# Kernel optimization log

Hardware: AMD Instinct MI355X
Metric: run time of the kernel (lower is better)

## Reference

```python
import jax, jax.numpy as jnp
import numpy as np

GENES = 20000   # input gene nodes (depth 0)
LEVEL = 10000   # nodes per subsequent depth level
STEPS = 7       # depth propagation steps
DEG = 16        # in-degree per dst node
N = GENES + STEPS * LEVEL          # 90000 total nodes
EPS = LEVEL * DEG                  # 160000 edges per step
E = STEPS * EPS                    # 1120000 total edges
B = 256
C = 2


def setup_inputs() -> dict:
    key = jax.random.key(0)
    k0, k1, k2 = jax.random.split(key, 3)
    X = jax.random.normal(k0, (B, GENES), jnp.float32)
    gene_map = jnp.arange(GENES, dtype=jnp.int32)

    rng = np.random.default_rng(0)
    src_list, dstu_list = [], []
    for k in range(STEPS):
        lo = 0 if k == 0 else GENES + (k - 1) * LEVEL
        hi = GENES if k == 0 else lo + LEVEL
        src_list.append(rng.integers(lo, hi, size=EPS))
        dstu_list.append(np.arange(GENES + k * LEVEL, GENES + (k + 1) * LEVEL))
    src = jnp.asarray(np.stack(src_list), dtype=jnp.int32)          # [STEPS, EPS]
    dst_unique = jnp.asarray(np.stack(dstu_list), dtype=jnp.int32)  # [STEPS, LEVEL]
    dst_pos = jnp.tile(jnp.repeat(jnp.arange(LEVEL, dtype=jnp.int32), DEG)[None, :], (STEPS, 1))
    eid = jnp.arange(E, dtype=jnp.int32).reshape(STEPS, EPS)
    root_ids = dst_unique[-1]

    edge_weight = jax.random.normal(k1, (E,), jnp.float32) * 0.01
    node_bias = jnp.zeros((N,), jnp.float32)
    head_W = jax.random.normal(k2, (LEVEL, C), jnp.float32) * (1.0 / np.sqrt(LEVEL))
    head_b = jnp.zeros((C,), jnp.float32)

    return dict(X=X, edge_weight=edge_weight, node_bias=node_bias,
                head_W=head_W, head_b=head_b, gene_map=gene_map,
                src=src, dst_pos=dst_pos, dst_unique=dst_unique,
                eid=eid, root_ids=root_ids)


def reference(X, edge_weight, node_bias, head_W, head_b,
              gene_map, src, dst_pos, dst_unique, eid, root_ids):
    # dropout is identity (eval mode / p=0)
    b = X.shape[0]
    h = jnp.zeros((b, N), X.dtype).at[:, gene_map].set(X)
    for k in range(src.shape[0]):  # fixed small number of depth steps
        w = edge_weight[eid[k]]                                   # [EPS]
        msg = h[:, src[k]] * w[None, :]                           # gather + scale [B, EPS]
        agg = jnp.zeros((b, dst_unique.shape[1]), h.dtype).at[:, dst_pos[k]].add(msg)
        h_dst = jnp.tanh(agg + node_bias[dst_unique[k]][None, :])  # [B, LEVEL]
        h = h.at[:, dst_unique[k]].set(h_dst)
    roots = h[:, root_ids]                                        # [B, LEVEL]
    return roots @ head_W + head_b
```

## Files before the change

kernel.cpp:

```cpp
#include <hip/hip_runtime.h>
#include <math.h>

#define GENES 20000
#define LEVEL 10000
#define STEPS 7
#define DEG   16
#define EPSZ  (LEVEL * DEG)
#define CCOLS 32
#define NCHUNK 8
#define SBLK  157
#define NGT   625
#define MSTRIDE 18

typedef unsigned short bf8 __attribute__((ext_vector_type(8)));

__device__ inline float bf2f(unsigned short u) {
    union { unsigned u; float f; } c; c.u = ((unsigned)u) << 16; return c.f;
}
__device__ inline unsigned short f2bf(float x) {
    union { float f; unsigned u; } c; c.f = x;
    return (unsigned short)((c.u + 0x7fffu + ((c.u >> 16) & 1u)) >> 16);
}

__global__ __launch_bounds__(256) void transpose_k(const float* __restrict__ X,
                                                   const int*   __restrict__ gene_map,
                                                   unsigned short* __restrict__ XT) {
    __shared__ float tile[32][33];
    const int chunk = blockIdx.x;
    const int lo = threadIdx.x & 31, r = threadIdx.x >> 5;
    unsigned short* XTp = XT + (size_t)chunk * GENES * CCOLS;
    for (int i = 0; i < 4; ++i) {
        const int gt = blockIdx.y * 4 + i;
        if (gt >= NGT) break;
        const int g0 = gt * 32;
        if (i) __syncthreads();
#pragma unroll
        for (int j = 0; j < 4; ++j) {
            const int b = r + j * 8;
            tile[b][lo] = X[(size_t)(chunk * CCOLS + b) * GENES + g0 + lo];
        }
        __syncthreads();
#pragma unroll
        for (int j = 0; j < 4; ++j) {
            const int gr   = r + j * 8;
            const int node = gene_map[g0 + gr];
            XTp[(size_t)node * CCOLS + lo] = f2bf(tile[lo][gr]);
        }
    }
}

__global__ __launch_bounds__(256) void step_k(const unsigned short* __restrict__ hprev,
                                              unsigned short*       __restrict__ hcur,
                                              const int*   __restrict__ src_k,
                                              const float* __restrict__ w_k,
                                              const float* __restrict__ node_bias,
                                              const int*   __restrict__ dstu_k,
                                              int src_base, int prev_rows) {
    const int bid   = blockIdx.x;
    const int chunk = bid & 7;
    const int cb    = bid >> 3;
    const int tid   = threadIdx.x;

    __shared__ int   s_src[64 * MSTRIDE];
    __shared__ float s_w  [64 * MSTRIDE];

    {
        const int m4 = cb * 256 + tid;
        if (m4 < EPSZ / 4) {
            const int4   sv = reinterpret_cast<const int4*>(src_k)[m4];
            const float4 wv = reinterpret_cast<const float4*>(w_k)[m4];
            const int j = tid >> 2, i = (tid & 3) * 4;
            *reinterpret_cast<int4*>  (&s_src[j * MSTRIDE + i]) = sv;
            *reinterpret_cast<float4*>(&s_w  [j * MSTRIDE + i]) = wv;
        }
    }
    __syncthreads();

    const int wave = tid >> 6, lane = tid & 63;
    const int q    = lane >> 2;
    const int c8   = (lane & 3) * 8;
    const int j    = wave * 16 + q;
    const int dest = cb * 64 + j;
    if (dest >= LEVEL) return;

    const unsigned short* prev = hprev + (size_t)chunk * prev_rows * CCOLS;
    unsigned short*       curp = hcur + (size_t)chunk * LEVEL * CCOLS;

    const int4   s0 = *reinterpret_cast<const int4*>  (&s_src[j * MSTRIDE + 0]);
    const int4   s1 = *reinterpret_cast<const int4*>  (&s_src[j * MSTRIDE + 4]);
    const int4   s2 = *reinterpret_cast<const int4*>  (&s_src[j * MSTRIDE + 8]);
    const int4   s3 = *reinterpret_cast<const int4*>  (&s_src[j * MSTRIDE + 12]);
    const float4 w0 = *reinterpret_cast<const float4*>(&s_w  [j * MSTRIDE + 0]);
    const float4 w1 = *reinterpret_cast<const float4*>(&s_w  [j * MSTRIDE + 4]);
    const float4 w2 = *reinterpret_cast<const float4*>(&s_w  [j * MSTRIDE + 8]);
    const float4 w3 = *reinterpret_cast<const float4*>(&s_w  [j * MSTRIDE + 12]);

    float a0 = 0.f, a1 = 0.f, a2 = 0.f, a3 = 0.f, a4 = 0.f, a5 = 0.f, a6 = 0.f, a7 = 0.f;
#define ACC(sv, wv) { const int idx = (sv) - src_base;                                      \
    const bf8 v = *reinterpret_cast<const bf8*>(prev + (size_t)idx * CCOLS + c8);           \
    a0 = fmaf(bf2f(v[0]), (wv), a0); a1 = fmaf(bf2f(v[1]), (wv), a1);                       \
    a2 = fmaf(bf2f(v[2]), (wv), a2); a3 = fmaf(bf2f(v[3]), (wv), a3);                       \
    a4 = fmaf(bf2f(v[4]), (wv), a4); a5 = fmaf(bf2f(v[5]), (wv), a5);                       \
    a6 = fmaf(bf2f(v[6]), (wv), a6); a7 = fmaf(bf2f(v[7]), (wv), a7); }
    ACC(s0.x, w0.x) ACC(s0.y, w0.y) ACC(s0.z, w0.z) ACC(s0.w, w0.w)
    ACC(s1.x, w1.x) ACC(s1.y, w1.y) ACC(s1.z, w1.z) ACC(s1.w, w1.w)
    ACC(s2.x, w2.x) ACC(s2.y, w2.y) ACC(s2.z, w2.z) ACC(s2.w, w2.w)
    ACC(s3.x, w3.x) ACC(s3.y, w3.y) ACC(s3.z, w3.z) ACC(s3.w, w3.w)
#undef ACC
    const float bz = node_bias[dstu_k[dest]];
    bf8 o;
    o[0] = f2bf(tanhf(a0 + bz));
    o[1] = f2bf(tanhf(a1 + bz));
    o[2] = f2bf(tanhf(a2 + bz));
    o[3] = f2bf(tanhf(a3 + bz));
    o[4] = f2bf(tanhf(a4 + bz));
    o[5] = f2bf(tanhf(a5 + bz));
    o[6] = f2bf(tanhf(a6 + bz));
    o[7] = f2bf(tanhf(a7 + bz));
    *reinterpret_cast<bf8*>(curp + (size_t)dest * CCOLS + c8) = o;
}

__global__ __launch_bounds__(256) void step7_head_k(const unsigned short* __restrict__ hprev,
                                                    const int*   __restrict__ src_k,
                                                    const float* __restrict__ w_k,
                                                    const float* __restrict__ node_bias,
                                                    const int*   __restrict__ dstu_k,
                                                    const float* __restrict__ head_W,
                                                    float*       __restrict__ part,
                                                    int src_base) {
    const int bid   = blockIdx.x;
    const int chunk = bid & 7;
    const int cb    = bid >> 3;
    const int tid   = threadIdx.x;

    __shared__ int   s_src[64 * MSTRIDE];
    __shared__ float s_w  [64 * MSTRIDE];
    __shared__ float o_tile[64][33];
    __shared__ float s_W2[64][2];
    __shared__ float red[8][64];

    {
        const int m4 = cb * 256 + tid;
        if (m4 < EPSZ / 4) {
            const int4   sv = reinterpret_cast<const int4*>(src_k)[m4];
            const float4 wv = reinterpret_cast<const float4*>(w_k)[m4];
            const int j = tid >> 2, i = (tid & 3) * 4;
            *reinterpret_cast<int4*>  (&s_src[j * MSTRIDE + i]) = sv;
            *reinterpret_cast<float4*>(&s_w  [j * MSTRIDE + i]) = wv;
        }
    }
    if (tid < 32) {
        const int f4 = cb * 32 + tid;
        float4 wv = make_float4(0.f, 0.f, 0.f, 0.f);
        if (f4 < (LEVEL * 2) / 4) wv = reinterpret_cast<const float4*>(head_W)[f4];
        s_W2[tid * 2 + 0][0] = wv.x; s_W2[tid * 2 + 0][1] = wv.y;
        s_W2[tid * 2 + 1][0] = wv.z; s_W2[tid * 2 + 1][1] = wv.w;
    }
    __syncthreads();

    const int wave = tid >> 6, lane = tid & 63;
    const int q    = lane >> 2;
    const int c8   = (lane & 3) * 8;
    const int j    = wave * 16 + q;
    const int dest = cb * 64 + j;

    const unsigned short* prev = hprev + (size_t)chunk * LEVEL * CCOLS;

    float o0 = 0.f, o1 = 0.f, o2 = 0.f, o3 = 0.f, o4 = 0.f, o5 = 0.f, o6 = 0.f, o7 = 0.f;
    if (dest < LEVEL) {
        const int4   s0 = *reinterpret_cast<const int4*>  (&s_src[j * MSTRIDE + 0]);
        const int4   s1 = *reinterpret_cast<const int4*>  (&s_src[j * MSTRIDE + 4]);
        const int4   s2 = *reinterpret_cast<const int4*>  (&s_src[j * MSTRIDE + 8]);
        const int4   s3 = *reinterpret_cast<const int4*>  (&s_src[j * MSTRIDE + 12]);
        const float4 w0 = *reinterpret_cast<const float4*>(&s_w  [j * MSTRIDE + 0]);
        const float4 w1 = *reinterpret_cast<const float4*>(&s_w  [j * MSTRIDE + 4]);
        const float4 w2 = *reinterpret_cast<const float4*>(&s_w  [j * MSTRIDE + 8]);
        const float4 w3 = *reinterpret_cast<const float4*>(&s_w  [j * MSTRIDE + 12]);

        float a0 = 0.f, a1 = 0.f, a2 = 0.f, a3 = 0.f, a4 = 0.f, a5 = 0.f, a6 = 0.f, a7 = 0.f;
#define ACC(sv, wv) { const int idx = (sv) - src_base;                                      \
    const bf8 v = *reinterpret_cast<const bf8*>(prev + (size_t)idx * CCOLS + c8);           \
    a0 = fmaf(bf2f(v[0]), (wv), a0); a1 = fmaf(bf2f(v[1]), (wv), a1);                       \
    a2 = fmaf(bf2f(v[2]), (wv), a2); a3 = fmaf(bf2f(v[3]), (wv), a3);                       \
    a4 = fmaf(bf2f(v[4]), (wv), a4); a5 = fmaf(bf2f(v[5]), (wv), a5);                       \
    a6 = fmaf(bf2f(v[6]), (wv), a6); a7 = fmaf(bf2f(v[7]), (wv), a7); }
        ACC(s0.x, w0.x) ACC(s0.y, w0.y) ACC(s0.z, w0.z) ACC(s0.w, w0.w)
        ACC(s1.x, w1.x) ACC(s1.y, w1.y) ACC(s1.z, w1.z) ACC(s1.w, w1.w)
        ACC(s2.x, w2.x) ACC(s2.y, w2.y) ACC(s2.z, w2.z) ACC(s2.w, w2.w)
        ACC(s3.x, w3.x) ACC(s3.y, w3.y) ACC(s3.z, w3.z) ACC(s3.w, w3.w)
#undef ACC
        const float bz = node_bias[dstu_k[dest]];
        o0 = tanhf(a0 + bz); o1 = tanhf(a1 + bz); o2 = tanhf(a2 + bz); o3 = tanhf(a3 + bz);
        o4 = tanhf(a4 + bz); o5 = tanhf(a5 + bz); o6 = tanhf(a6 + bz); o7 = tanhf(a7 + bz);
    }
    o_tile[j][c8 + 0] = o0; o_tile[j][c8 + 1] = o1;
    o_tile[j][c8 + 2] = o2; o_tile[j][c8 + 3] = o3;
    o_tile[j][c8 + 4] = o4; o_tile[j][c8 + 5] = o5;
    o_tile[j][c8 + 6] = o6; o_tile[j][c8 + 7] = o7;
    __syncthreads();

    {
        const int col = tid & 31, slot = tid >> 5;
        float a0 = 0.f, a1 = 0.f;
#pragma unroll
        for (int e = 0; e < 8; ++e) {
            const int jj = slot * 8 + e;
            const float v = o_tile[jj][col];
            a0 = fmaf(v, s_W2[jj][0], a0);
            a1 = fmaf(v, s_W2[jj][1], a1);
        }
        red[slot][col * 2 + 0] = a0;
        red[slot][col * 2 + 1] = a1;
    }
    __syncthreads();
    if (tid < 64) {
        float s = 0.f;
#pragma unroll
        for (int p = 0; p < 8; ++p) s += red[p][tid];
        part[((size_t)chunk * SBLK + cb) * 64 + tid] = s;
    }
}

__global__ __launch_bounds__(64) void head_final_k(const float* __restrict__ part,
                                                   const float* __restrict__ head_b,
                                                   float*       __restrict__ out) {
    const int chunk = blockIdx.x;
    const int t     = threadIdx.x;
    float acc = head_b[t & 1];
    for (int q = 0; q < SBLK; ++q)
        acc += part[((size_t)chunk * SBLK + q) * 64 + t];
    out[chunk * 64 + t] = acc;
}

extern "C" void kernel_launch(void* const* d_in, const int* in_sizes, int n_in,
                              void* d_out, int out_size, void* d_ws, size_t ws_size,
                              hipStream_t stream) {
    const float* X           = (const float*)d_in[0];
    const float* edge_weight = (const float*)d_in[1];
    const float* node_bias   = (const float*)d_in[2];
    const float* head_W      = (const float*)d_in[3];
    const float* head_b      = (const float*)d_in[4];
    const int*   gene_map    = (const int*)  d_in[5];
    const int*   src         = (const int*)  d_in[6];
    const int*   dst_unique  = (const int*)  d_in[8];
    float* out = (float*)d_out;

    char* ws = (char*)d_ws;
    unsigned short* XT   = (unsigned short*)(ws);
    unsigned short* lvlA = (unsigned short*)(ws + 10240000);
    unsigned short* lvlB = (unsigned short*)(ws + 15360000);
    float*          part = (float*)         (ws + 20480000);

    transpose_k<<<dim3(NCHUNK, 157), 256, 0, stream>>>(X, gene_map, XT);

    unsigned short* bufs[2] = {lvlA, lvlB};
    for (int k = 0; k < STEPS - 1; ++k) {
        const unsigned short* hprev = (k == 0) ? XT : bufs[(k - 1) & 1];
        const int prevrows = (k == 0) ? GENES : LEVEL;
        const int srcbase  = (k == 0) ? 0 : GENES + (k - 1) * LEVEL;
        step_k<<<SBLK * NCHUNK, 256, 0, stream>>>(hprev, bufs[k & 1],
                                                  src + (size_t)k * EPSZ,
                                                  edge_weight + (size_t)k * EPSZ,
                                                  node_bias,
                                                  dst_unique + (size_t)k * LEVEL,
                                                  srcbase, prevrows);
    }

    {
        const int k = STEPS - 1;
        const unsigned short* hprev = bufs[(k - 1) & 1];
        const int srcbase = GENES + (k - 1) * LEVEL;
        step7_head_k<<<SBLK * NCHUNK, 256, 0, stream>>>(hprev,
                                                        src + (size_t)k * EPSZ,
                                                        edge_weight + (size_t)k * EPSZ,
                                                        node_bias,
                                                        dst_unique + (size_t)k * LEVEL,
                                                        head_W, part, srcbase);
        head_final_k<<<NCHUNK, 64, 0, stream>>>(part, head_b, out);
    }
    (void)in_sizes; (void)n_in; (void)out_size; (void)ws_size;
}
```

Before: 91.68 us.

## Split each destination's edges across two lanes and vectorize transpose loads

The step kernel now handles 32 destinations per block instead of 64 and splits each destination's 16 incoming edges across two lane groups. Each lane issues 8 independent gathers up front and the halves are combined with a shuffle-xor reduction, doubling the block count to raise memory-level parallelism and latency hiding. The transpose kernel reads X with float4 loads instead of scalar loads. The cost is extra shuffles, more blocks, and half the lanes idling during the tanh and store epilogue.

```diff
diff --git a/kernel.cpp b/kernel.cpp
--- a/kernel.cpp
+++ b/kernel.cpp
@@ -9,6 +9,7 @@
 #define CCOLS 32
 #define NCHUNK 8
 #define SBLK  157
+#define DBLK  313
 #define NGT   625
 #define MSTRIDE 18
 
@@ -27,22 +28,26 @@
                                                    unsigned short* __restrict__ XT) {
     __shared__ float tile[32][33];
     const int chunk = blockIdx.x;
-    const int lo = threadIdx.x & 31, r = threadIdx.x >> 5;
+    const int l4  = threadIdx.x & 7;
+    const int r8  = threadIdx.x >> 3;
+    const int lo  = threadIdx.x & 31;
+    const int gr8 = threadIdx.x >> 5;
     unsigned short* XTp = XT + (size_t)chunk * GENES * CCOLS;
     for (int i = 0; i < 4; ++i) {
         const int gt = blockIdx.y * 4 + i;
         if (gt >= NGT) break;
         const int g0 = gt * 32;
         if (i) __syncthreads();
-#pragma unroll
-        for (int j = 0; j < 4; ++j) {
-            const int b = r + j * 8;
-            tile[b][lo] = X[(size_t)(chunk * CCOLS + b) * GENES + g0 + lo];
-        }
+        const float4 xv = *reinterpret_cast<const float4*>(
+            X + (size_t)(chunk * CCOLS + r8) * GENES + g0 + l4 * 4);
+        tile[r8][l4 * 4 + 0] = xv.x;
+        tile[r8][l4 * 4 + 1] = xv.y;
+        tile[r8][l4 * 4 + 2] = xv.z;
+        tile[r8][l4 * 4 + 3] = xv.w;
         __syncthreads();
 #pragma unroll
-        for (int j = 0; j < 4; ++j) {
-            const int gr   = r + j * 8;
+        for (int jj = 0; jj < 4; ++jj) {
+            const int gr   = gr8 + jj * 8;
             const int node = gene_map[g0 + gr];
             XTp[(size_t)node * CCOLS + lo] = f2bf(tile[lo][gr]);
         }
@@ -61,63 +66,84 @@
     const int cb    = bid >> 3;
     const int tid   = threadIdx.x;
 
-    __shared__ int   s_src[64 * MSTRIDE];
-    __shared__ float s_w  [64 * MSTRIDE];
-
-    {
-        const int m4 = cb * 256 + tid;
+    __shared__ int   s_src[32 * MSTRIDE];
+    __shared__ float s_w  [32 * MSTRIDE];
+
+    if (tid < 128) {
+        const int m4 = cb * 128 + tid;
         if (m4 < EPSZ / 4) {
-            const int4   sv = reinterpret_cast<const int4*>(src_k)[m4];
+            const int4 sv = reinterpret_cast<const int4*>(src_k)[m4];
+            const int j = tid >> 2, i = (tid & 3) * 4;
+            *reinterpret_cast<int4*>(&s_src[j * MSTRIDE + i]) = sv;
+        }
+    } else {
+        const int t  = tid - 128;
+        const int m4 = cb * 128 + t;
+        if (m4 < EPSZ / 4) {
             const float4 wv = reinterpret_cast<const float4*>(w_k)[m4];
-            const int j = tid >> 2, i = (tid & 3) * 4;
-            *reinterpret_cast<int4*>  (&s_src[j * MSTRIDE + i]) = sv;
-            *reinterpret_cast<float4*>(&s_w  [j * MSTRIDE + i]) = wv;
+            const int j = t >> 2, i = (t & 3) * 4;
+            *reinterpret_cast<float4*>(&s_w[j * MSTRIDE + i]) = wv;
         }
     }
     __syncthreads();
 
     const int wave = tid >> 6, lane = tid & 63;
-    const int q    = lane >> 2;
-    const int c8   = (lane & 3) * 8;
-    const int j    = wave * 16 + q;
-    const int dest = cb * 64 + j;
-    if (dest >= LEVEL) return;
-
-    const unsigned short* prev = hprev + (size_t)chunk * prev_rows * CCOLS;
-    unsigned short*       curp = hcur + (size_t)chunk * LEVEL * CCOLS;
-
-    const int4   s0 = *reinterpret_cast<const int4*>  (&s_src[j * MSTRIDE + 0]);
-    const int4   s1 = *reinterpret_cast<const int4*>  (&s_src[j * MSTRIDE + 4]);
-    const int4   s2 = *reinterpret_cast<const int4*>  (&s_src[j * MSTRIDE + 8]);
-    const int4   s3 = *reinterpret_cast<const int4*>  (&s_src[j * MSTRIDE + 12]);
-    const float4 w0 = *reinterpret_cast<const float4*>(&s_w  [j * MSTRIDE + 0]);
-    const float4 w1 = *reinterpret_cast<const float4*>(&s_w  [j * MSTRIDE + 4]);
-    const float4 w2 = *reinterpret_cast<const float4*>(&s_w  [j * MSTRIDE + 8]);
-    const float4 w3 = *reinterpret_cast<const float4*>(&s_w  [j * MSTRIDE + 12]);
-
-    float a0 = 0.f, a1 = 0.f, a2 = 0.f, a3 = 0.f, a4 = 0.f, a5 = 0.f, a6 = 0.f, a7 = 0.f;
-#define ACC(sv, wv) { const int idx = (sv) - src_base;                                      \
-    const bf8 v = *reinterpret_cast<const bf8*>(prev + (size_t)idx * CCOLS + c8);           \
-    a0 = fmaf(bf2f(v[0]), (wv), a0); a1 = fmaf(bf2f(v[1]), (wv), a1);                       \
-    a2 = fmaf(bf2f(v[2]), (wv), a2); a3 = fmaf(bf2f(v[3]), (wv), a3);                       \
-    a4 = fmaf(bf2f(v[4]), (wv), a4); a5 = fmaf(bf2f(v[5]), (wv), a5);                       \
-    a6 = fmaf(bf2f(v[6]), (wv), a6); a7 = fmaf(bf2f(v[7]), (wv), a7); }
-    ACC(s0.x, w0.x) ACC(s0.y, w0.y) ACC(s0.z, w0.z) ACC(s0.w, w0.w)
-    ACC(s1.x, w1.x) ACC(s1.y, w1.y) ACC(s1.z, w1.z) ACC(s1.w, w1.w)
-    ACC(s2.x, w2.x) ACC(s2.y, w2.y) ACC(s2.z, w2.z) ACC(s2.w, w2.w)
-    ACC(s3.x, w3.x) ACC(s3.y, w3.y) ACC(s3.z, w3.z) ACC(s3.w, w3.w)
-#undef ACC
-    const float bz = node_bias[dstu_k[dest]];
-    bf8 o;
-    o[0] = f2bf(tanhf(a0 + bz));
-    o[1] = f2bf(tanhf(a1 + bz));
-    o[2] = f2bf(tanhf(a2 + bz));
-    o[3] = f2bf(tanhf(a3 + bz));
-    o[4] = f2bf(tanhf(a4 + bz));
-    o[5] = f2bf(tanhf(a5 + bz));
-    o[6] = f2bf(tanhf(a6 + bz));
-    o[7] = f2bf(tanhf(a7 + bz));
-    *reinterpret_cast<bf8*>(curp + (size_t)dest * CCOLS + c8) = o;
+    const int c2 = lane & 3;
+    const int eh = (lane >> 2) & 1;
+    const int q  = lane >> 3;
+    const int j  = wave * 8 + q;
+    const int dest = cb * 32 + j;
+    const int c8 = c2 * 8;
+
+    if (dest < LEVEL) {
+        const unsigned short* prev = hprev + (size_t)chunk * prev_rows * CCOLS;
+        unsigned short*       curp = hcur + (size_t)chunk * LEVEL * CCOLS;
+
+        const int mb = j * MSTRIDE + eh * 8;
+        const int4   sA = *reinterpret_cast<const int4*>  (&s_src[mb]);
+        const int4   sB = *reinterpret_cast<const int4*>  (&s_src[mb + 4]);
+        const float4 wA = *reinterpret_cast<const float4*>(&s_w  [mb]);
+        const float4 wB = *reinterpret_cast<const float4*>(&s_w  [mb + 4]);
+
+#define GL(sv) (*reinterpret_cast<const bf8*>(prev + (size_t)((sv) - src_base) * CCOLS + c8))
+        const bf8 v0 = GL(sA.x);
+        const bf8 v1 = GL(sA.y);
+        const bf8 v2 = GL(sA.z);
+        const bf8 v3 = GL(sA.w);
+        const bf8 v4 = GL(sB.x);
+        const bf8 v5 = GL(sB.y);
+        const bf8 v6 = GL(sB.z);
+        const bf8 v7 = GL(sB.w);
+#undef GL
+
+        float a0 = 0.f, a1 = 0.f, a2 = 0.f, a3 = 0.f, a4 = 0.f, a5 = 0.f, a6 = 0.f, a7 = 0.f;
+#define FMA8(v, wv) { a0 = fmaf(bf2f((v)[0]), (wv), a0); a1 = fmaf(bf2f((v)[1]), (wv), a1);  \
+                      a2 = fmaf(bf2f((v)[2]), (wv), a2); a3 = fmaf(bf2f((v)[3]), (wv), a3);  \
+                      a4 = fmaf(bf2f((v)[4]), (wv), a4); a5 = fmaf(bf2f((v)[5]), (wv), a5);  \
+                      a6 = fmaf(bf2f((v)[6]), (wv), a6); a7 = fmaf(bf2f((v)[7]), (wv), a7); }
+        FMA8(v0, wA.x) FMA8(v1, wA.y) FMA8(v2, wA.z) FMA8(v3, wA.w)
+        FMA8(v4, wB.x) FMA8(v5, wB.y) FMA8(v6, wB.z) FMA8(v7, wB.w)
+#undef FMA8
+
+        a0 += __shfl_xor(a0, 4); a1 += __shfl_xor(a1, 4);
+        a2 += __shfl_xor(a2, 4); a3 += __shfl_xor(a3, 4);
+        a4 += __shfl_xor(a4, 4); a5 += __shfl_xor(a5, 4);
+        a6 += __shfl_xor(a6, 4); a7 += __shfl_xor(a7, 4);
+
+        if (eh == 0) {
+            const float bz = node_bias[dstu_k[dest]];
+            bf8 o;
+            o[0] = f2bf(tanhf(a0 + bz));
+            o[1] = f2bf(tanhf(a1 + bz));
+            o[2] = f2bf(tanhf(a2 + bz));
+            o[3] = f2bf(tanhf(a3 + bz));
+            o[4] = f2bf(tanhf(a4 + bz));
+            o[5] = f2bf(tanhf(a5 + bz));
+            o[6] = f2bf(tanhf(a6 + bz));
+            o[7] = f2bf(tanhf(a7 + bz));
+            *reinterpret_cast<bf8*>(curp + (size_t)dest * CCOLS + c8) = o;
+        }
+    }
 }
 
 __global__ __launch_bounds__(256) void step7_head_k(const unsigned short* __restrict__ hprev,
@@ -258,7 +284,7 @@
         const unsigned short* hprev = (k == 0) ? XT : bufs[(k - 1) & 1];
         const int prevrows = (k == 0) ? GENES : LEVEL;
         const int srcbase  = (k == 0) ? 0 : GENES + (k - 1) * LEVEL;
-        step_k<<<SBLK * NCHUNK, 256, 0, stream>>>(hprev, bufs[k & 1],
+        step_k<<<DBLK * NCHUNK, 256, 0, stream>>>(hprev, bufs[k & 1],
                                                   src + (size_t)k * EPSZ,
                                                   edge_weight + (size_t)k * EPSZ,
                                                   node_bias,
```

Result: no change. 91.31 us (-0.4%).
